# Kernel tuning notes

Hardware: AMD Instinct MI355X
Metric: run time of the kernel (lower is better)

## Reference

```python
import itertools
import jax, jax.numpy as jnp
import numpy as np

B, S, H = 1, 2048, 1024
NH, KVH, HD = 16, 8, 64
E, TOPK, I = 8, 2, 3584
EPS = 1e-6
THETA = 1000000.0
COMBS = np.array(list(itertools.combinations(range(E), TOPK)), dtype=np.int32)  # [28,2]


def setup_inputs() -> dict:
    key = jax.random.key(0)
    ks = jax.random.split(key, 12)
    s = 0.02
    return {
        "hidden_states": jax.random.normal(ks[0], (B, S, H), jnp.float32),
        "ln1_w": jnp.ones((H,), jnp.float32),
        "ln2_w": jnp.ones((H,), jnp.float32),
        "wq": jax.random.normal(ks[1], (NH * HD, H), jnp.float32) * s,
        "wk": jax.random.normal(ks[2], (KVH * HD, H), jnp.float32) * s,
        "wv": jax.random.normal(ks[3], (KVH * HD, H), jnp.float32) * s,
        "wo": jax.random.normal(ks[4], (H, NH * HD), jnp.float32) * s,
        "gate_w": jax.random.normal(ks[5], (E, H), jnp.float32) * s,
        "w1": jax.random.normal(ks[6], (E, I, H), jnp.float32) * s,
        "w2": jax.random.normal(ks[7], (E, H, I), jnp.float32) * s,
        "w3": jax.random.normal(ks[8], (E, I, H), jnp.float32) * s,
    }


def _rmsnorm(x, w):
    v = x.astype(jnp.float32)
    v = v * jax.lax.rsqrt(jnp.mean(v * v, axis=-1, keepdims=True) + EPS)
    return (w * v).astype(x.dtype)


def _rotate_half(x):
    h = x.shape[-1] // 2
    return jnp.concatenate([-x[..., h:], x[..., :h]], axis=-1)


def reference(hidden_states, ln1_w, ln2_w, wq, wk, wv, wo, gate_w, w1, w2, w3):
    residual = hidden_states
    x = _rmsnorm(hidden_states, ln1_w)

    # --- Mixtral attention (GQA + RoPE, causal) ---
    q = (x @ wq.T).reshape(B, S, NH, HD).transpose(0, 2, 1, 3)   # [B,NH,S,HD]
    k = (x @ wk.T).reshape(B, S, KVH, HD).transpose(0, 2, 1, 3)  # [B,KVH,S,HD]
    v = (x @ wv.T).reshape(B, S, KVH, HD).transpose(0, 2, 1, 3)

    pos = jnp.arange(S, dtype=jnp.float32)
    inv_freq = 1.0 / (THETA ** (jnp.arange(0, HD, 2, dtype=jnp.float32) / HD))
    freqs = pos[:, None] * inv_freq[None, :]               # [S,HD/2]
    emb = jnp.concatenate([freqs, freqs], axis=-1)          # [S,HD]
    cos, sin = jnp.cos(emb)[None, None], jnp.sin(emb)[None, None]
    q = q * cos + _rotate_half(q) * sin
    k = k * cos + _rotate_half(k) * sin

    rep = NH // KVH
    k = jnp.repeat(k, rep, axis=1)
    v = jnp.repeat(v, rep, axis=1)

    scores = jnp.einsum("bhsd,bhtd->bhst", q, k) / jnp.sqrt(jnp.float32(HD))
    causal = jnp.tril(jnp.ones((S, S), dtype=bool))
    scores = jnp.where(causal[None, None], scores, jnp.finfo(jnp.float32).min)
    attn = jax.nn.softmax(scores.astype(jnp.float32), axis=-1).astype(q.dtype)
    ctx = jnp.einsum("bhst,bhtd->bhsd", attn, v)
    ctx = ctx.transpose(0, 2, 1, 3).reshape(B, S, NH * HD)
    hidden_states = residual + ctx @ wo.T

    # --- MoE block (combination routing, no experts_used mask) ---
    residual = hidden_states
    x = _rmsnorm(hidden_states, ln2_w).reshape(-1, H)       # [N,H], N=B*S
    N = x.shape[0]
    router_logits = x @ gate_w.T                            # [N,E]
    rw = jax.nn.softmax(router_logits.astype(jnp.float32), axis=-1)

    combs = jnp.asarray(COMBS)                              # [28,2]
    comb_scores = jnp.take(rw, combs, axis=1).sum(-1)       # [N,28]
    sel = jnp.argmax(comb_scores, axis=-1)                  # [N]
    selected_experts = combs[sel]                           # [N,TOPK]
    w = jnp.take_along_axis(rw, selected_experts, axis=1)   # [N,TOPK]
    w = (w / w.sum(-1, keepdims=True)).astype(x.dtype)

    # per-token per-expert combine weights (0 if not selected)
    wm = jnp.zeros((N, E), x.dtype).at[jnp.arange(N)[:, None], selected_experts].set(w)

    # dense evaluation of all experts, combined by sparse weights
    h1 = jax.nn.silu(jnp.einsum("nh,eih->nei", x, w1))
    h3 = jnp.einsum("nh,eih->nei", x, w3)
    out_e = jnp.einsum("nei,ehi->neh", h1 * h3, w2)          # [N,E,H]
    moe_out = jnp.einsum("neh,ne->nh", out_e, wm)

    hidden_states = residual + moe_out.reshape(B, S, H)
    return hidden_states
```

## Files before the change

### kernel.cpp

```cpp
#include <hip/hip_runtime.h>
#include <hip/hip_bf16.h>
#include <math.h>

constexpr int S_ = 2048, H_ = 1024, NH_ = 16, KVH_ = 8, HD_ = 64;
constexpr int E_ = 8, I_ = 3584;
constexpr int KSLC = 4;
constexpr float EPS_ = 1e-6f;
constexpr float THETA_ = 1000000.0f;

#define SDIV(a,b) (((a)+(b)-1)/(b))

typedef __attribute__((ext_vector_type(8))) short bf16x8;
typedef __attribute__((ext_vector_type(4))) float f32x4;

__device__ inline unsigned pkbf(float a, float b) {
    unsigned r;
    asm("v_cvt_pk_bf16_f32 %0, %1, %2" : "=v"(r) : "v"(a), "v"(b));
    return r;
}
__device__ inline unsigned short f2bf(float f) {
    unsigned u = __float_as_uint(f);
    u += 0x7FFF + ((u >> 16) & 1);
    return (unsigned short)(u >> 16);
}
__device__ inline float bf2f(unsigned short v) {
    return __uint_as_float((unsigned)v << 16);
}

__device__ inline void gload16u(const void* gsrc, char* ldsArr, int uoff) {
    int off = __builtin_amdgcn_readfirstlane(uoff);
    __builtin_amdgcn_global_load_lds(
        (__attribute__((address_space(1))) void*)(gsrc),
        (__attribute__((address_space(3))) void*)(ldsArr + off), 16, 0, 0);
}
__device__ inline void vmdrain() {
    asm volatile("s_waitcnt vmcnt(0)" ::: "memory");
}

template<bool WB>
__device__ inline int4 loadW16(const void* W, size_t elemOff) {
    if constexpr (WB) {
        return *(const int4*)((const unsigned short*)W + elemOff);
    } else {
        const float* s = (const float*)W + elemOff;
        float4 f0 = *(const float4*)s, f1 = *(const float4*)(s + 4);
        return make_int4(pkbf(f0.x, f0.y), pkbf(f0.z, f0.w),
                         pkbf(f1.x, f1.y), pkbf(f1.z, f1.w));
    }
}

__global__ __launch_bounds__(256) void conv_bf16(const float* __restrict__ in,
                                                 unsigned short* __restrict__ out, long n8)
{
    long i = (long)blockIdx.x * 256 + threadIdx.x;
    long stride = (long)gridDim.x * 256;
    for (; i < n8; i += stride) {
        const float* s = in + i * 8;
        float4 f0 = *(const float4*)s, f1 = *(const float4*)(s + 4);
        *(int4*)(out + i * 8) = make_int4(pkbf(f0.x, f0.y), pkbf(f0.z, f0.w),
                                          pkbf(f1.x, f1.y), pkbf(f1.z, f1.w));
    }
}

__global__ __launch_bounds__(256) void rmsnorm_k(const float* __restrict__ x,
                                                 const float* __restrict__ w,
                                                 float* __restrict__ out,
                                                 unsigned short* __restrict__ outb)
{
    int row = blockIdx.x;
    int tid = threadIdx.x;
    const float* xr = x + (size_t)row * H_;
    float4 v = *(const float4*)&xr[tid * 4];
    float ss = v.x*v.x + v.y*v.y + v.z*v.z + v.w*v.w;
#pragma unroll
    for (int off = 32; off > 0; off >>= 1) ss += __shfl_xor(ss, off);
    __shared__ float red[4];
    if ((tid & 63) == 0) red[tid >> 6] = ss;
    __syncthreads();
    float tot = red[0] + red[1] + red[2] + red[3];
    float r = rsqrtf(tot / (float)H_ + EPS_);
    float4 wv = *(const float4*)&w[tid * 4];
    float4 o;
    o.x = v.x * r * wv.x; o.y = v.y * r * wv.y;
    o.z = v.z * r * wv.z; o.w = v.w * r * wv.w;
    *(float4*)&out[(size_t)row * H_ + tid * 4] = o;
    if (outb) {
        uint2 pk = make_uint2(pkbf(o.x, o.y), pkbf(o.z, o.w));
        *(uint2*)&outb[(size_t)row * H_ + tid * 4] = pk;
    }
}

template<bool OUTF32>
__global__ __launch_bounds__(256) void dense_g(const unsigned short* __restrict__ A,
                                               const unsigned short* __restrict__ B,
                                               const float* __restrict__ Res,
                                               void* __restrict__ C,
                                               int K, int ldC)
{
    int m0 = blockIdx.y * 128, n0 = blockIdx.x * 64;
    int tid = threadIdx.x;
    __shared__ char As[16384], Bs[8192];
    int lane = tid & 63, w = tid >> 6, wm = w >> 1, wn = w & 1;
    int lm = lane & 15, lk = lane >> 4;
    int wb16 = (tid & ~63) * 16;

    f32x4 z = {0.f, 0.f, 0.f, 0.f};
    f32x4 acc[4][2];
#pragma unroll
    for (int mf = 0; mf < 4; ++mf)
#pragma unroll
        for (int nf = 0; nf < 2; ++nf) acc[mf][nf] = z;

    for (int kt = 0; kt < K / 64; ++kt) {
        int kb = kt * 64;
#pragma unroll
        for (int it = 0; it < 4; ++it) {
            int g = tid + it * 256, row = g >> 3, kg = g & 7;
            int kgs = kg ^ (row & 7);
            gload16u(A + (size_t)(m0 + row) * K + kb + kgs * 8, As, wb16 + it * 4096);
        }
#pragma unroll
        for (int it = 0; it < 2; ++it) {
            int g = tid + it * 256, row = g >> 3, kg = g & 7;
            int kgs = kg ^ (row & 7);
            gload16u(B + (size_t)(n0 + row) * K + kb + kgs * 8, Bs, wb16 + it * 4096);
        }
        vmdrain();
        __syncthreads();
#pragma unroll
        for (int ks = 0; ks < 2; ++ks) {
            bf16x8 af[4];
#pragma unroll
            for (int mf = 0; mf < 4; ++mf) {
                int row = wm * 64 + mf * 16 + lm;
                af[mf] = *(const bf16x8*)(As + row * 128 + ((ks * 64 + lk * 16) ^ ((row & 7) << 4)));
            }
#pragma unroll
            for (int nf = 0; nf < 2; ++nf) {
                int brow = wn * 32 + nf * 16 + lm;
                bf16x8 bf = *(const bf16x8*)(Bs + brow * 128 + ((ks * 64 + lk * 16) ^ ((brow & 7) << 4)));
#pragma unroll
                for (int mf = 0; mf < 4; ++mf)
                    acc[mf][nf] = __builtin_amdgcn_mfma_f32_16x16x32_bf16(af[mf], bf, acc[mf][nf], 0, 0, 0);
            }
        }
        __syncthreads();
    }

#pragma unroll
    for (int mf = 0; mf < 4; ++mf)
#pragma unroll
        for (int nf = 0; nf < 2; ++nf) {
            int col = n0 + wn * 32 + nf * 16 + lm;
#pragma unroll
            for (int j = 0; j < 4; ++j) {
                int row = m0 + wm * 64 + mf * 16 + lk * 4 + j;
                float v = acc[mf][nf][j];
                if constexpr (OUTF32) {
                    float r = Res ? Res[(size_t)row * ldC + col] : 0.0f;
                    ((float*)C)[(size_t)row * ldC + col] = v + r;
                } else {
                    ((unsigned short*)C)[(size_t)row * ldC + col] = f2bf(v);
                }
            }
        }
}

template<bool WB>
__global__ __launch_bounds__(256) void dense_mfma(const float* __restrict__ A,
                                                  const void* __restrict__ Bw,
                                                  const float* __restrict__ Res,
                                                  float* __restrict__ C,
                                                  int M, int N, int K)
{
    __shared__ char As[16384], Bs[16384];
    int tid = threadIdx.x;
    int m0 = blockIdx.y * 128, n0 = blockIdx.x * 128;
    int lane = tid & 63, w = tid >> 6, wm = w >> 1, wn = w & 1;
    int lm = lane & 15, lk = lane >> 4;

    int4 rA[4], rB[4];
    auto loadAll = [&](int kb) {
#pragma unroll
        for (int it = 0; it < 4; ++it) {
            int g = tid + it * 256, row = g >> 3, kg = g & 7;
            const float* s = A + (size_t)(m0 + row) * K + kb + kg * 8;
            float4 f0 = *(const float4*)s, f1 = *(const float4*)(s + 4);
            rA[it] = make_int4(pkbf(f0.x, f0.y), pkbf(f0.z, f0.w),
                               pkbf(f1.x, f1.y), pkbf(f1.z, f1.w));
            rB[it] = loadW16<WB>(Bw, (size_t)(n0 + row) * K + kb + kg * 8);
        }
    };
    auto writeAll = [&]() {
#pragma unroll
        for (int it = 0; it < 4; ++it) {
            int g = tid + it * 256, row = g >> 3, kg = g & 7;
            int byte = row * 128 + ((kg * 16) ^ ((row & 7) << 4));
            *(int4*)(As + byte) = rA[it];
            *(int4*)(Bs + byte) = rB[it];
        }
    };

    f32x4 z = {0.f, 0.f, 0.f, 0.f};
    f32x4 acc[4][4];
#pragma unroll
    for (int mf = 0; mf < 4; ++mf)
#pragma unroll
        for (int nf = 0; nf < 4; ++nf) acc[mf][nf] = z;

    loadAll(0);
    for (int kt = 0; kt < K / 64; ++kt) {
        __syncthreads();
        writeAll();
        __syncthreads();
        if (kt + 1 < K / 64) loadAll((kt + 1) * 64);
#pragma unroll
        for (int ks = 0; ks < 2; ++ks) {
            bf16x8 af[4];
#pragma unroll
            for (int mf = 0; mf < 4; ++mf) {
                int row = wm * 64 + mf * 16 + lm;
                af[mf] = *(const bf16x8*)(As + row * 128 + ((ks * 64 + lk * 16) ^ ((row & 7) << 4)));
            }
#pragma unroll
            for (int nf = 0; nf < 4; ++nf) {
                int brow = wn * 64 + nf * 16 + lm;
                bf16x8 bf = *(const bf16x8*)(Bs + brow * 128 + ((ks * 64 + lk * 16) ^ ((brow & 7) << 4)));
#pragma unroll
                for (int mf = 0; mf < 4; ++mf)
                    acc[mf][nf] = __builtin_amdgcn_mfma_f32_16x16x32_bf16(af[mf], bf, acc[mf][nf], 0, 0, 0);
            }
        }
    }

#pragma unroll
    for (int mf = 0; mf < 4; ++mf)
#pragma unroll
        for (int nf = 0; nf < 4; ++nf) {
            int col = n0 + wn * 64 + nf * 16 + lm;
#pragma unroll
            for (int j = 0; j < 4; ++j) {
                int row = m0 + wm * 64 + mf * 16 + lk * 4 + j;
                float r = Res ? Res[(size_t)row * N + col] : 0.0f;
                C[(size_t)row * N + col] = acc[mf][nf][j] + r;
            }
        }
}

__global__ __launch_bounds__(256) void rope_conv_b(const unsigned short* __restrict__ qkvb,
                                                   unsigned short* __restrict__ qbf,
                                                   unsigned short* __restrict__ kbf)
{
    int idx = blockIdx.x * 256 + threadIdx.x;
    const int totq = S_ * NH_ * 32;
    const int tot = totq + S_ * KVH_ * 32;
    if (idx >= tot) return;
    const unsigned short* src; unsigned short* dst; int s, di; float sc;
    if (idx < totq) {
        s = idx / (NH_ * 32); int r = idx % (NH_ * 32); int h = r >> 5;
        src = qkvb + (size_t)s * 2048 + h * 64;
        dst = qbf + ((size_t)s * NH_ + h) * HD_;
        di = r & 31; sc = 0.125f;
    } else {
        int j2 = idx - totq;
        s = j2 / (KVH_ * 32); int r = j2 % (KVH_ * 32); int kvh = r >> 5;
        src = qkvb + (size_t)s * 2048 + 1024 + kvh * 64;
        dst = kbf + ((size_t)s * KVH_ + kvh) * HD_;
        di = r & 31; sc = 1.0f;
    }
    float invf = powf(THETA_, -(2.0f * di) / (float)HD_);
    float ang = (float)s * invf;
    float c = cosf(ang), sn = sinf(ang);
    float x0 = bf2f(src[di]), x1 = bf2f(src[di + 32]);
    dst[di]      = f2bf((x0 * c - x1 * sn) * sc);
    dst[di + 32] = f2bf((x1 * c + x0 * sn) * sc);
}

__global__ __launch_bounds__(256) void v_trans_b(const unsigned short* __restrict__ qkvb,
                                                 unsigned short* __restrict__ vtb)
{
    int t0 = blockIdx.x * 64, kvh = blockIdx.y;
    __shared__ unsigned short T[64][64];
    int tid = threadIdx.x;
    int k = tid >> 2, d0 = (tid & 3) * 16;
    const unsigned short* src = qkvb + (size_t)(t0 + k) * 2048 + 1536 + kvh * 64 + d0;
    *(int4*)&T[k][d0]     = *(const int4*)(src);
    *(int4*)&T[k][d0 + 8] = *(const int4*)(src + 8);
    __syncthreads();
    int d = tid >> 2, s0 = (tid & 3) * 16;
    unsigned short tmp[16] __attribute__((aligned(16)));
#pragma unroll
    for (int x = 0; x < 16; ++x) {
        int s = s0 + x;
        int key = 16 * (s & 3) + (s >> 2);
        tmp[x] = T[key][d];
    }
    unsigned short* dst = vtb + ((size_t)kvh * HD_ + d) * S_ + t0 + s0;
    *(int4*)(dst)     = *(int4*)(tmp);
    *(int4*)(dst + 8) = *(int4*)(tmp + 8);
}

__global__ __launch_bounds__(256) void rope_conv(const float* __restrict__ q,
                                                 const float* __restrict__ k,
                                                 unsigned short* __restrict__ qbf,
                                                 unsigned short* __restrict__ kbf)
{
    int idx = blockIdx.x * 256 + threadIdx.x;
    const int totq = S_ * NH_ * 32;
    const int tot = totq + S_ * KVH_ * 32;
    if (idx >= tot) return;
    const float* base; unsigned short* obase; int s, di; float sc;
    if (idx < totq) {
        s = idx / (NH_ * 32); int r = idx % (NH_ * 32);
        size_t o = ((size_t)s * NH_ + (r >> 5)) * HD_;
        base = q + o; obase = qbf + o; di = r & 31; sc = 0.125f;
    } else {
        int j2 = idx - totq;
        s = j2 / (KVH_ * 32); int r = j2 % (KVH_ * 32);
        size_t o = ((size_t)s * KVH_ + (r >> 5)) * HD_;
        base = k + o; obase = kbf + o; di = r & 31; sc = 1.0f;
    }
    float invf = powf(THETA_, -(2.0f * di) / (float)HD_);
    float ang = (float)s * invf;
    float c = cosf(ang), sn = sinf(ang);
    float x0 = base[di], x1 = base[di + 32];
    obase[di]      = f2bf((x0 * c - x1 * sn) * sc);
    obase[di + 32] = f2bf((x1 * c + x0 * sn) * sc);
}

__global__ __launch_bounds__(256) void v_trans(const float* __restrict__ v,
                                               unsigned short* __restrict__ vtb)
{
    int t0 = blockIdx.x * 64, kvh = blockIdx.y;
    __shared__ unsigned short T[64][64];
    int tid = threadIdx.x;
    int k = tid >> 2, d0 = (tid & 3) * 16;
    const float* src = v + ((size_t)(t0 + k) * KVH_ + kvh) * HD_ + d0;
#pragma unroll
    for (int x = 0; x < 4; ++x) {
        float4 f = *(const float4*)(src + x * 4);
        T[k][d0 + x*4 + 0] = f2bf(f.x);
        T[k][d0 + x*4 + 1] = f2bf(f.y);
        T[k][d0 + x*4 + 2] = f2bf(f.z);
        T[k][d0 + x*4 + 3] = f2bf(f.w);
    }
    __syncthreads();
    int d = tid >> 2, s0 = (tid & 3) * 16;
    unsigned short tmp[16] __attribute__((aligned(16)));
#pragma unroll
    for (int x = 0; x < 16; ++x) {
        int s = s0 + x;
        int key = 16 * (s & 3) + (s >> 2);
        tmp[x] = T[key][d];
    }
    unsigned short* dst = vtb + ((size_t)kvh * HD_ + d) * S_ + t0 + s0;
    *(int4*)(dst)     = *(int4*)(tmp);
    *(int4*)(dst + 8) = *(int4*)(tmp + 8);
}

__global__ __launch_bounds__(256) void attn_mfma(const unsigned short* __restrict__ qbf,
                                                 const unsigned short* __restrict__ kbf,
                                                 const unsigned short* __restrict__ vtb,
                                                 float* __restrict__ ctx,
                                                 unsigned short* __restrict__ ctxb)
{
    __shared__ char Ps[4 * 2048];
    int pair = blockIdx.x, h = blockIdx.y, z = blockIdx.z;
    int qb = z ? (31 - pair) : pair;
    int q0 = qb * 64;
    int kvh = h >> 1;
    int tid = threadIdx.x;
    int w = tid >> 6, lane = tid & 63;
    int lm = lane & 15, lk = lane >> 4;
    char* myP = Ps + w * 2048;

    bf16x8 qf[2];
    const unsigned short* qrow = qbf + ((size_t)(q0 + w * 16 + lm) * NH_ + h) * HD_;
#pragma unroll
    for (int ks = 0; ks < 2; ++ks)
        qf[ks] = *(const bf16x8*)(qrow + ks * 32 + lk * 8);

    float m_[4], l_[4];
    f32x4 o_[4];
#pragma unroll
    for (int j = 0; j < 4; ++j) { m_[j] = -1e30f; l_[j] = 0.f; }
    f32x4 zf = {0.f, 0.f, 0.f, 0.f};
#pragma unroll
    for (int nd = 0; nd < 4; ++nd) o_[nd] = zf;

    for (int t0 = 0; t0 <= q0; t0 += 64) {
        f32x4 s[4];
#pragma unroll
        for (int nf = 0; nf < 4; ++nf) {
            const unsigned short* krow = kbf + ((size_t)(t0 + nf * 16 + lm) * KVH_ + kvh) * HD_;
            bf16x8 k0 = *(const bf16x8*)(krow + lk * 8);
            bf16x8 k1 = *(const bf16x8*)(krow + 32 + lk * 8);
            f32x4 acc = zf;
            acc = __builtin_amdgcn_mfma_f32_16x16x32_bf16(qf[0], k0, acc, 0, 0, 0);
            acc = __builtin_amdgcn_mfma_f32_16x16x32_bf16(qf[1], k1, acc, 0, 0, 0);
            s[nf] = acc;
        }
        if (t0 == q0) {
#pragma unroll
            for (int nf = 0; nf < 4; ++nf)
#pragma unroll
                for (int j = 0; j < 4; ++j) {
                    int key = nf * 16 + lm, qq = w * 16 + lk * 4 + j;
                    if (key > qq) s[nf][j] = -1e30f;
                }
        }
        float p_[4][4];
#pragma unroll
        for (int j = 0; j < 4; ++j) {
            float mx = fmaxf(fmaxf(s[0][j], s[1][j]), fmaxf(s[2][j], s[3][j]));
#pragma unroll
            for (int off = 8; off > 0; off >>= 1) mx = fmaxf(mx, __shfl_xor(mx, off));
            float nm = fmaxf(m_[j], mx);
            float rs = __expf(m_[j] - nm);
            float sum = 0.f;
#pragma unroll
            for (int nf = 0; nf < 4; ++nf) {
                float pv = __expf(s[nf][j] - nm);
                p_[nf][j] = pv; sum += pv;
            }
#pragma unroll
            for (int off = 8; off > 0; off >>= 1) sum += __shfl_xor(sum, off);
            l_[j] = l_[j] * rs + sum;
            m_[j] = nm;
#pragma unroll
            for (int nd = 0; nd < 4; ++nd) o_[nd][j] *= rs;
        }
#pragma unroll
        for (int j = 0; j < 4; ++j) {
            int r = lk * 4 + j;
            unsigned lo = pkbf(p_[0][j], p_[1][j]);
            unsigned hi = pkbf(p_[2][j], p_[3][j]);
            int byte = (lm * 8) ^ ((r & 7) << 4);
            *(uint2*)(myP + r * 128 + byte) = make_uint2(lo, hi);
        }
#pragma unroll
        for (int ks = 0; ks < 2; ++ks) {
            int byte = (ks * 64 + lk * 16) ^ ((lm & 7) << 4);
            bf16x8 pA = *(const bf16x8*)(myP + lm * 128 + byte);
#pragma unroll
            for (int nd = 0; nd < 4; ++nd) {
                const unsigned short* vrow = vtb + ((size_t)kvh * HD_ + nd * 16 + lm) * S_ + t0 + ks * 32 + lk * 8;
                bf16x8 vB = *(const bf16x8*)vrow;
                o_[nd] = __builtin_amdgcn_mfma_f32_16x16x32_bf16(pA, vB, o_[nd], 0, 0, 0);
            }
        }
    }
#pragma unroll
    for (int nd = 0; nd < 4; ++nd)
#pragma unroll
        for (int j = 0; j < 4; ++j) {
            int r = lk * 4 + j;
            float val = o_[nd][j] / l_[j];
            size_t oidx = ((size_t)(q0 + w * 16 + r) * NH_ + h) * HD_ + nd * 16 + lm;
            ctx[oidx] = val;
            ctxb[oidx] = f2bf(val);
        }
}

__global__ __launch_bounds__(64) void router_k(const float* __restrict__ x2,
                                               const float* __restrict__ gw,
                                               int* __restrict__ cnt,
                                               int* __restrict__ elist,
                                               int* __restrict__ eslot,
                                               float* __restrict__ wslot)
{
    int n = blockIdx.x, lane = threadIdx.x;
    float part[E_];
#pragma unroll
    for (int e = 0; e < E_; ++e) part[e] = 0.f;
    const float* xr = x2 + (size_t)n * H_;
    for (int j = lane; j < H_; j += 64) {
        float xv = xr[j];
#pragma unroll
        for (int e = 0; e < E_; ++e) part[e] = fmaf(xv, gw[e * H_ + j], part[e]);
    }
#pragma unroll
    for (int e = 0; e < E_; ++e)
#pragma unroll
        for (int off = 32; off > 0; off >>= 1) part[e] += __shfl_xor(part[e], off);
    if (lane == 0) {
        float mx = part[0];
#pragma unroll
        for (int e = 1; e < E_; ++e) mx = fmaxf(mx, part[e]);
        float rw[E_]; float ssum = 0.f;
#pragma unroll
        for (int e = 0; e < E_; ++e) { rw[e] = expf(part[e] - mx); ssum += rw[e]; }
#pragma unroll
        for (int e = 0; e < E_; ++e) rw[e] /= ssum;
        float best = -1.f; int ba = 0, bb = 1;
        for (int a = 0; a < E_; ++a)
            for (int b = a + 1; b < E_; ++b) {
                float scv = rw[a] + rw[b];
                if (scv > best) { best = scv; ba = a; bb = b; }
            }
        float wa = rw[ba], wb = rw[bb], wsum = wa + wb;
        wa /= wsum; wb /= wsum;
        int p = atomicAdd(&cnt[ba], 1);
        elist[ba * S_ + p] = n; eslot[ba * S_ + p] = 2 * n;
        p = atomicAdd(&cnt[bb], 1);
        elist[bb * S_ + p] = n; eslot[bb * S_ + p] = 2 * n + 1;
        wslot[2 * n] = wa; wslot[2 * n + 1] = wb;
    }
}

__global__ __launch_bounds__(256) void moe_up_g(const unsigned short* __restrict__ x2b,
                                                const unsigned short* __restrict__ w1b,
                                                const unsigned short* __restrict__ w3b,
                                                const int* __restrict__ cnt,
                                                const int* __restrict__ elist,
                                                const int* __restrict__ eslot,
                                                unsigned short* __restrict__ hbuf)
{
    int e = blockIdx.z;
    int c = cnt[e];
    int p0 = blockIdx.y * 128;
    if (p0 >= c) return;
    int i0 = blockIdx.x * 64;
    int tid = threadIdx.x;

    __shared__ char As[16384], B1s[8192], B3s[8192];
    __shared__ int rowtokS[128], rowslotS[128];
    if (tid < 128) {
        int p = min(p0 + tid, c - 1);
        rowtokS[tid]  = elist[e * S_ + p];
        rowslotS[tid] = eslot[e * S_ + p];
    }
    __syncthreads();

    int lane = tid & 63, w = tid >> 6, wm = w >> 1, wn = w & 1;
    int lm = lane & 15, lk = lane >> 4;
    int wb16 = (tid & ~63) * 16;
    size_t wbase = (size_t)e * I_ * H_;

    f32x4 z = {0.f, 0.f, 0.f, 0.f};
    f32x4 acc1[4][2], acc3[4][2];
#pragma unroll
    for (int mf = 0; mf < 4; ++mf)
#pragma unroll
        for (int nf = 0; nf < 2; ++nf) { acc1[mf][nf] = z; acc3[mf][nf] = z; }

    for (int kt = 0; kt < H_ / 64; ++kt) {
        int kb = kt * 64;
#pragma unroll
        for (int it = 0; it < 4; ++it) {
            int g = tid + it * 256, row = g >> 3, kg = g & 7;
            int kgs = kg ^ (row & 7);
            gload16u(x2b + (size_t)rowtokS[row] * H_ + kb + kgs * 8, As, wb16 + it * 4096);
        }
#pragma unroll
        for (int it = 0; it < 2; ++it) {
            int g = tid + it * 256, row = g >> 3, kg = g & 7;
            int kgs = kg ^ (row & 7);
            size_t off = wbase + (size_t)(i0 + row) * H_ + kb + kgs * 8;
            gload16u(w1b + off, B1s, wb16 + it * 4096);
            gload16u(w3b + off, B3s, wb16 + it * 4096);
        }
        vmdrain();
        __syncthreads();
#pragma unroll
        for (int ks = 0; ks < 2; ++ks) {
            bf16x8 af[4];
#pragma unroll
            for (int mf = 0; mf < 4; ++mf) {
                int row = wm * 64 + mf * 16 + lm;
                af[mf] = *(const bf16x8*)(As + row * 128 + ((ks * 64 + lk * 16) ^ ((row & 7) << 4)));
            }
#pragma unroll
            for (int nf = 0; nf < 2; ++nf) {
                int brow = wn * 32 + nf * 16 + lm;
                int bby = brow * 128 + ((ks * 64 + lk * 16) ^ ((brow & 7) << 4));
                bf16x8 b1 = *(const bf16x8*)(B1s + bby);
                bf16x8 b3 = *(const bf16x8*)(B3s + bby);
#pragma unroll
                for (int mf = 0; mf < 4; ++mf) {
                    acc1[mf][nf] = __builtin_amdgcn_mfma_f32_16x16x32_bf16(af[mf], b1, acc1[mf][nf], 0, 0, 0);
                    acc3[mf][nf] = __builtin_amdgcn_mfma_f32_16x16x32_bf16(af[mf], b3, acc3[mf][nf], 0, 0, 0);
                }
            }
        }
        __syncthreads();
    }

#pragma unroll
    for (int mf = 0; mf < 4; ++mf)
#pragma unroll
        for (int nf = 0; nf < 2; ++nf) {
            int coli = i0 + wn * 32 + nf * 16 + lm;
#pragma unroll
            for (int j = 0; j < 4; ++j) {
                int rloc = wm * 64 + mf * 16 + lk * 4 + j;
                if (p0 + rloc < c) {
                    float h1 = acc1[mf][nf][j];
                    float val = h1 / (1.f + __expf(-h1)) * acc3[mf][nf][j];
                    hbuf[(size_t)rowslotS[rloc] * I_ + coli] = f2bf(val);
                }
            }
        }
}

__global__ __launch_bounds__(256) void moe_dn_g(const unsigned short* __restrict__ hbuf,
                                                const unsigned short* __restrict__ w2b,
                                                const int* __restrict__ cnt,
                                                const int* __restrict__ eslot,
                                                unsigned short* __restrict__ dbuf)
{
    int e = blockIdx.z >> 2;
    int slice = blockIdx.z & 3;
    int c = cnt[e];
    int p0 = blockIdx.y * 128;
    if (p0 >= c) return;
    int h0 = blockIdx.x * 128;
    int tid = threadIdx.x;
    const int kb0 = slice * (I_ / KSLC);

    __shared__ char As[16384], Bs[16384];
    __shared__ int rowslotS[128];
    if (tid < 128) rowslotS[tid] = eslot[e * S_ + min(p0 + tid, c - 1)];
    __syncthreads();

    int lane = tid & 63, w = tid >> 6, wm = w >> 1, wn = w & 1;
    int lm = lane & 15, lk = lane >> 4;
    int wb16 = (tid & ~63) * 16;
    size_t wbase = (size_t)e * H_ * I_;

    f32x4 z = {0.f, 0.f, 0.f, 0.f};
    f32x4 acc[4][4];
#pragma unroll
    for (int mf = 0; mf < 4; ++mf)
#pragma unroll
        for (int nf = 0; nf < 4; ++nf) acc[mf][nf] = z;

    const int NKT = (I_ / KSLC) / 64;
    for (int kt = 0; kt < NKT; ++kt) {
        int kb = kb0 + kt * 64;
#pragma unroll
        for (int it = 0; it < 4; ++it) {
            int g = tid + it * 256, row = g >> 3, kg = g & 7;
            int kgs = kg ^ (row & 7);
            gload16u(hbuf + (size_t)rowslotS[row] * I_ + kb + kgs * 8, As, wb16 + it * 4096);
            gload16u(w2b + wbase + (size_t)(h0 + row) * I_ + kb + kgs * 8, Bs, wb16 + it * 4096);
        }
        vmdrain();
        __syncthreads();
#pragma unroll
        for (int ks = 0; ks < 2; ++ks) {
            bf16x8 af[4];
#pragma unroll
            for (int mf = 0; mf < 4; ++mf) {
                int row = wm * 64 + mf * 16 + lm;
                af[mf] = *(const bf16x8*)(As + row * 128 + ((ks * 64 + lk * 16) ^ ((row & 7) << 4)));
            }
#pragma unroll
            for (int nf = 0; nf < 4; ++nf) {
                int brow = wn * 64 + nf * 16 + lm;
                bf16x8 bf = *(const bf16x8*)(Bs + brow * 128 + ((ks * 64 + lk * 16) ^ ((brow & 7) << 4)));
#pragma unroll
                for (int mf = 0; mf < 4; ++mf)
                    acc[mf][nf] = __builtin_amdgcn_mfma_f32_16x16x32_bf16(af[mf], bf, acc[mf][nf], 0, 0, 0);
            }
        }
        __syncthreads();
    }

    unsigned short* dslice = dbuf + (size_t)slice * S_ * 2 * H_;
#pragma unroll
    for (int mf = 0; mf < 4; ++mf)
#pragma unroll
        for (int nf = 0; nf < 4; ++nf) {
            int colh = h0 + wn * 64 + nf * 16 + lm;
#pragma unroll
            for (int j = 0; j < 4; ++j) {
                int rloc = wm * 64 + mf * 16 + lk * 4 + j;
                if (p0 + rloc < c)
                    dslice[(size_t)rowslotS[rloc] * H_ + colh] = f2bf(acc[mf][nf][j]);
            }
        }
}

template<bool WB>
__global__ __launch_bounds__(256) void moe_up_mfma(const float* __restrict__ x2,
                                                   const void* __restrict__ w1,
                                                   const void* __restrict__ w3,
                                                   const int* __restrict__ cnt,
                                                   const int* __restrict__ elist,
                                                   const int* __restrict__ eslot,
                                                   unsigned short* __restrict__ hbuf)
{
    int e = blockIdx.z;
    int c = cnt[e];
    int p0 = blockIdx.y * 128;
    if (p0 >= c) return;
    int i0 = blockIdx.x * 64;
    int tid = threadIdx.x;

    __shared__ char As[16384], B1s[8192], B3s[8192];
    __shared__ int rowtokS[128], rowslotS[128];
    if (tid < 128) {
        int p = min(p0 + tid, c - 1);
        rowtokS[tid]  = elist[e * S_ + p];
        rowslotS[tid] = eslot[e * S_ + p];
    }
    __syncthreads();

    int lane = tid & 63, w = tid >> 6, wm = w >> 1, wn = w & 1;
    int lm = lane & 15, lk = lane >> 4;
    size_t wbase = (size_t)e * I_ * H_;

    int4 rA[4], rB1[2], rB3[2];
    auto loadAll = [&](int kb) {
#pragma unroll
        for (int it = 0; it < 4; ++it) {
            int g = tid + it * 256, row = g >> 3, kg = g & 7;
            const float* s = x2 + (size_t)rowtokS[row] * H_ + kb + kg * 8;
            float4 f0 = *(const float4*)s, f1 = *(const float4*)(s + 4);
            rA[it] = make_int4(pkbf(f0.x, f0.y), pkbf(f0.z, f0.w),
                               pkbf(f1.x, f1.y), pkbf(f1.z, f1.w));
        }
#pragma unroll
        for (int it = 0; it < 2; ++it) {
            int g = tid + it * 256, row = g >> 3, kg = g & 7;
            size_t off = wbase + (size_t)(i0 + row) * H_ + kb + kg * 8;
            rB1[it] = loadW16<WB>(w1, off);
            rB3[it] = loadW16<WB>(w3, off);
        }
    };
    auto writeAll = [&]() {
#pragma unroll
        for (int it = 0; it < 4; ++it) {
            int g = tid + it * 256, row = g >> 3, kg = g & 7;
            int byte = row * 128 + ((kg * 16) ^ ((row & 7) << 4));
            *(int4*)(As + byte) = rA[it];
        }
#pragma unroll
        for (int it = 0; it < 2; ++it) {
            int g = tid + it * 256, row = g >> 3, kg = g & 7;
            int byte = row * 128 + ((kg * 16) ^ ((row & 7) << 4));
            *(int4*)(B1s + byte) = rB1[it];
            *(int4*)(B3s + byte) = rB3[it];
        }
    };

    f32x4 z = {0.f, 0.f, 0.f, 0.f};
    f32x4 acc1[4][2], acc3[4][2];
#pragma unroll
    for (int mf = 0; mf < 4; ++mf)
#pragma unroll
        for (int nf = 0; nf < 2; ++nf) { acc1[mf][nf] = z; acc3[mf][nf] = z; }

    loadAll(0);
    for (int kt = 0; kt < H_ / 64; ++kt) {
        __syncthreads();
        writeAll();
        __syncthreads();
        if (kt + 1 < H_ / 64) loadAll((kt + 1) * 64);
#pragma unroll
        for (int ks = 0; ks < 2; ++ks) {
            bf16x8 af[4];
#pragma unroll
            for (int mf = 0; mf < 4; ++mf) {
                int row = wm * 64 + mf * 16 + lm;
                af[mf] = *(const bf16x8*)(As + row * 128 + ((ks * 64 + lk * 16) ^ ((row & 7) << 4)));
            }
#pragma unroll
            for (int nf = 0; nf < 2; ++nf) {
                int brow = wn * 32 + nf * 16 + lm;
                int bby = brow * 128 + ((ks * 64 + lk * 16) ^ ((brow & 7) << 4));
                bf16x8 b1 = *(const bf16x8*)(B1s + bby);
                bf16x8 b3 = *(const bf16x8*)(B3s + bby);
#pragma unroll
                for (int mf = 0; mf < 4; ++mf) {
                    acc1[mf][nf] = __builtin_amdgcn_mfma_f32_16x16x32_bf16(af[mf], b1, acc1[mf][nf], 0, 0, 0);
                    acc3[mf][nf] = __builtin_amdgcn_mfma_f32_16x16x32_bf16(af[mf], b3, acc3[mf][nf], 0, 0, 0);
                }
            }
        }
    }

#pragma unroll
    for (int mf = 0; mf < 4; ++mf)
#pragma unroll
        for (int nf = 0; nf < 2; ++nf) {
            int coli = i0 + wn * 32 + nf * 16 + lm;
#pragma unroll
            for (int j = 0; j < 4; ++j) {
                int rloc = wm * 64 + mf * 16 + lk * 4 + j;
                if (p0 + rloc < c) {
                    float h1 = acc1[mf][nf][j];
                    float val = h1 / (1.f + __expf(-h1)) * acc3[mf][nf][j];
                    hbuf[(size_t)rowslotS[rloc] * I_ + coli] = f2bf(val);
                }
            }
        }
}

template<bool WB>
__global__ __launch_bounds__(256) void moe_dn_mfma(const unsigned short* __restrict__ hbuf,
                                                   const void* __restrict__ w2,
                                                   const int* __restrict__ cnt,
                                                   const int* __restrict__ eslot,
                                                   unsigned short* __restrict__ dbuf)
{
    int e = blockIdx.z >> 2;
    int slice = blockIdx.z & 3;
    int c = cnt[e];
    int p0 = blockIdx.y * 128;
    if (p0 >= c) return;
    int h0 = blockIdx.x * 128;
    int tid = threadIdx.x;
    const int kb0 = slice * (I_ / KSLC);

    __shared__ char As[16384], Bs[16384];
    __shared__ int rowslotS[128];
    if (tid < 128) rowslotS[tid] = eslot[e * S_ + min(p0 + tid, c - 1)];
    __syncthreads();

    int lane = tid & 63, w = tid >> 6, wm = w >> 1, wn = w & 1;
    int lm = lane & 15, lk = lane >> 4;
    size_t wbase = (size_t)e * H_ * I_;

    int4 rA[4], rB[4];
    auto loadAll = [&](int kb) {
#pragma unroll
        for (int it = 0; it < 4; ++it) {
            int g = tid + it * 256, row = g >> 3, kg = g & 7;
            rA[it] = *(const int4*)(hbuf + (size_t)rowslotS[row] * I_ + kb + kg * 8);
            rB[it] = loadW16<WB>(w2, wbase + (size_t)(h0 + row) * I_ + kb + kg * 8);
        }
    };
    auto writeAll = [&]() {
#pragma unroll
        for (int it = 0; it < 4; ++it) {
            int g = tid + it * 256, row = g >> 3, kg = g & 7;
            int byte = row * 128 + ((kg * 16) ^ ((row & 7) << 4));
            *(int4*)(As + byte) = rA[it];
            *(int4*)(Bs + byte) = rB[it];
        }
    };

    f32x4 z = {0.f, 0.f, 0.f, 0.f};
    f32x4 acc[4][4];
#pragma unroll
    for (int mf = 0; mf < 4; ++mf)
#pragma unroll
        for (int nf = 0; nf < 4; ++nf) acc[mf][nf] = z;

    loadAll(kb0);
    const int NKT = (I_ / KSLC) / 64;
    for (int kt = 0; kt < NKT; ++kt) {
        __syncthreads();
        writeAll();
        __syncthreads();
        if (kt + 1 < NKT) loadAll(kb0 + (kt + 1) * 64);
#pragma unroll
        for (int ks = 0; ks < 2; ++ks) {
            bf16x8 af[4];
#pragma unroll
            for (int mf = 0; mf < 4; ++mf) {
                int row = wm * 64 + mf * 16 + lm;
                af[mf] = *(const bf16x8*)(As + row * 128 + ((ks * 64 + lk * 16) ^ ((row & 7) << 4)));
            }
#pragma unroll
            for (int nf = 0; nf < 4; ++nf) {
                int brow = wn * 64 + nf * 16 + lm;
                bf16x8 bf = *(const bf16x8*)(Bs + brow * 128 + ((ks * 64 + lk * 16) ^ ((brow & 7) << 4)));
#pragma unroll
                for (int mf = 0; mf < 4; ++mf)
                    acc[mf][nf] = __builtin_amdgcn_mfma_f32_16x16x32_bf16(af[mf], bf, acc[mf][nf], 0, 0, 0);
            }
        }
    }

    unsigned short* dslice = dbuf + (size_t)slice * S_ * 2 * H_;
#pragma unroll
    for (int mf = 0; mf < 4; ++mf)
#pragma unroll
        for (int nf = 0; nf < 4; ++nf) {
            int colh = h0 + wn * 64 + nf * 16 + lm;
#pragma unroll
            for (int j = 0; j < 4; ++j) {
                int rloc = wm * 64 + mf * 16 + lk * 4 + j;
                if (p0 + rloc < c)
                    dslice[(size_t)rowslotS[rloc] * H_ + colh] = f2bf(acc[mf][nf][j]);
            }
        }
}

__global__ __launch_bounds__(256) void combine_k(const float* __restrict__ hid2,
                                                 const unsigned short* __restrict__ dbuf,
                                                 const float* __restrict__ wslot,
                                                 float* __restrict__ out)
{
    int idx = blockIdx.x * 256 + threadIdx.x;
    if (idx >= S_ * H_) return;
    int n = idx >> 10;
    int hcol = idx & (H_ - 1);
    float s0 = 0.f, s1 = 0.f;
#pragma unroll
    for (int sl = 0; sl < KSLC; ++sl) {
        const unsigned short* base = dbuf + (size_t)sl * S_ * 2 * H_;
        s0 += bf2f(base[(size_t)(2 * n)     * H_ + hcol]);
        s1 += bf2f(base[(size_t)(2 * n + 1) * H_ + hcol]);
    }
    out[idx] = hid2[idx] + wslot[2 * n] * s0 + wslot[2 * n + 1] * s1;
}

extern "C" void kernel_launch(void* const* d_in, const int* in_sizes, int n_in,
                              void* d_out, int out_size, void* d_ws, size_t ws_size,
                              hipStream_t stream)
{
    const float* hidden = (const float*)d_in[0];
    const float* ln1    = (const float*)d_in[1];
    const float* ln2    = (const float*)d_in[2];
    const float* wq     = (const float*)d_in[3];
    const float* wk     = (const float*)d_in[4];
    const float* wv     = (const float*)d_in[5];
    const float* wo     = (const float*)d_in[6];
    const float* gw     = (const float*)d_in[7];
    const float* w1     = (const float*)d_in[8];
    const float* w2     = (const float*)d_in[9];
    const float* w3     = (const float*)d_in[10];
    float* out = (float*)d_out;

    char* p = (char*)d_ws;
    auto alignp = [&]() { p = (char*)(((uintptr_t)p + 255) & ~(uintptr_t)255); };
    auto alloc_f = [&](size_t n) { alignp(); float* r = (float*)p; p += n * 4; return r; };
    auto alloc_h = [&](size_t n) { alignp(); unsigned short* r = (unsigned short*)p; p += n * 2; return r; };
    auto alloc_i = [&](size_t n) { alignp(); int* r = (int*)p; p += n * 4; return r; };

    float* xb   = alloc_f((size_t)S_ * H_);
    unsigned short* xbb = alloc_h((size_t)S_ * H_);
    float* q    = alloc_f((size_t)S_ * NH_ * HD_);
    float* kb   = alloc_f((size_t)S_ * KVH_ * HD_);
    float* vb   = alloc_f((size_t)S_ * KVH_ * HD_);
    unsigned short* qkvb = alloc_h((size_t)S_ * 2048);
    float* hid2 = alloc_f((size_t)S_ * H_);
    float* x2   = alloc_f((size_t)S_ * H_);
    unsigned short* x2b  = alloc_h((size_t)S_ * H_);
    unsigned short* ctxb = alloc_h((size_t)S_ * H_);
    unsigned short* hbuf = alloc_h((size_t)S_ * 2 * I_);
    unsigned short* dbuf = alloc_h((size_t)KSLC * S_ * 2 * H_);
    float* wslot= alloc_f((size_t)S_ * 2);
    unsigned short* qbf = alloc_h((size_t)S_ * NH_ * HD_);
    unsigned short* kbf = alloc_h((size_t)S_ * KVH_ * HD_);
    unsigned short* vtb = alloc_h((size_t)KVH_ * HD_ * S_);
    int* cnt   = alloc_i(E_);
    int* elist = alloc_i((size_t)E_ * S_);
    int* eslot = alloc_i((size_t)E_ * S_);
    float* ctx = xb;

    size_t used = (size_t)(p - (char*)d_ws);
    const size_t nW = (size_t)E_ * I_ * H_;
    size_t wbf_bytes = (3 * nW + (size_t)2048 * H_ + (size_t)H_ * NH_ * HD_) * 2 + 8192;
    bool WB = ws_size > used && (ws_size - used) >= wbf_bytes;

    unsigned short *w1b = nullptr, *w3b = nullptr, *w2b = nullptr;
    unsigned short *wqkvb = nullptr, *wob = nullptr;
    if (WB) {
        w1b = alloc_h(nW); w3b = alloc_h(nW); w2b = alloc_h(nW);
        wqkvb = alloc_h((size_t)2048 * H_);
        wob = alloc_h((size_t)H_ * NH_ * HD_);
    }

    hipMemsetAsync(cnt, 0, E_ * sizeof(int), stream);

    if (WB) {
        conv_bf16<<<2048, 256, 0, stream>>>(w1, w1b, (long)(nW / 8));
        conv_bf16<<<2048, 256, 0, stream>>>(w3, w3b, (long)(nW / 8));
        conv_bf16<<<2048, 256, 0, stream>>>(w2, w2b, (long)(nW / 8));
        conv_bf16<<<512, 256, 0, stream>>>(wq, wqkvb, (long)((size_t)NH_*HD_*H_ / 8));
        conv_bf16<<<256, 256, 0, stream>>>(wk, wqkvb + (size_t)NH_*HD_*H_, (long)((size_t)KVH_*HD_*H_ / 8));
        conv_bf16<<<256, 256, 0, stream>>>(wv, wqkvb + (size_t)(NH_+KVH_)*HD_*H_, (long)((size_t)KVH_*HD_*H_ / 8));
        conv_bf16<<<512, 256, 0, stream>>>(wo, wob, (long)((size_t)H_*NH_*HD_ / 8));
    }

    rmsnorm_k<<<S_, 256, 0, stream>>>(hidden, ln1, xb, WB ? xbb : nullptr);

    if (WB) {
        dense_g<false><<<dim3(32, 16), 256, 0, stream>>>(xbb, wqkvb, nullptr, qkvb, H_, 2048);
        {
            int tot = S_ * (NH_ + KVH_) * 32;
            rope_conv_b<<<SDIV(tot, 256), 256, 0, stream>>>(qkvb, qbf, kbf);
        }
        v_trans_b<<<dim3(S_ / 64, KVH_), 256, 0, stream>>>(qkvb, vtb);
        attn_mfma<<<dim3(16, NH_, 2), 256, 0, stream>>>(qbf, kbf, vtb, ctx, ctxb);
        dense_g<true><<<dim3(16, 16), 256, 0, stream>>>(ctxb, wob, hidden, hid2, H_, H_);
    } else {
        dense_mfma<false><<<dim3(8, 16), 256, 0, stream>>>(xb, wq, nullptr, q,  S_, NH_ * HD_, H_);
        dense_mfma<false><<<dim3(4, 16), 256, 0, stream>>>(xb, wk, nullptr, kb, S_, KVH_ * HD_, H_);
        dense_mfma<false><<<dim3(4, 16), 256, 0, stream>>>(xb, wv, nullptr, vb, S_, KVH_ * HD_, H_);
        {
            int tot = S_ * (NH_ + KVH_) * 32;
            rope_conv<<<SDIV(tot, 256), 256, 0, stream>>>(q, kb, qbf, kbf);
        }
        v_trans<<<dim3(S_ / 64, KVH_), 256, 0, stream>>>(vb, vtb);
        attn_mfma<<<dim3(16, NH_, 2), 256, 0, stream>>>(qbf, kbf, vtb, ctx, ctxb);
        dense_mfma<false><<<dim3(8, 16), 256, 0, stream>>>(ctx, wo, hidden, hid2, S_, H_, NH_ * HD_);
    }

    rmsnorm_k<<<S_, 256, 0, stream>>>(hid2, ln2, x2, x2b);
    router_k<<<S_, 64, 0, stream>>>(x2, gw, cnt, elist, eslot, wslot);

    if (WB) {
        moe_up_g<<<dim3(I_ / 64, S_ / 128, E_), 256, 0, stream>>>(x2b, w1b, w3b, cnt, elist, eslot, hbuf);
        moe_dn_g<<<dim3(H_ / 128, S_ / 128, E_ * KSLC), 256, 0, stream>>>(hbuf, w2b, cnt, eslot, dbuf);
    } else {
        moe_up_mfma<false><<<dim3(I_ / 64, S_ / 128, E_), 256, 0, stream>>>(x2, w1, w3, cnt, elist, eslot, hbuf);
        moe_dn_mfma<false><<<dim3(H_ / 128, S_ / 128, E_ * KSLC), 256, 0, stream>>>(hbuf, w2, cnt, eslot, dbuf);
    }
    combine_k<<<SDIV(S_ * H_, 256), 256, 0, stream>>>(hid2, dbuf, wslot, out);
}
```

Before: 467.5 us.

## Double-buffer LDS tiles in MoE up and down GEMM kernels

Both MoE GEMM kernels (up-projection with w1/w3 and down-projection with w2) now keep two LDS buffers. The next K tile is loaded into the spare buffer while MFMAs run on the current one, and one barrier per iteration is removed. The aim is to hide global-to-LDS load latency behind compute. In exchange, LDS use per block doubles (64KB for both kernels), which can lower occupancy. The WAR hazard is covered by the single barrier after vmdrain, since the stage for kt+1 writes the buffer last read in kt-1.

Result: slower. 524.4 us (+12.2%).

```diff
diff --git a/kernel.cpp b/kernel.cpp
--- a/kernel.cpp
+++ b/kernel.cpp
@@ -523,7 +523,7 @@
     int i0 = blockIdx.x * 64;
     int tid = threadIdx.x;
 
-    __shared__ char As[16384], B1s[8192], B3s[8192];
+    __shared__ char As[2][16384], B1s[2][8192], B3s[2][8192];
     __shared__ int rowtokS[128], rowslotS[128];
     if (tid < 128) {
         int p = min(p0 + tid, c - 1);
@@ -537,6 +537,24 @@
     int wb16 = (tid & ~63) * 16;
     size_t wbase = (size_t)e * I_ * H_;
 
+    auto stage = [&](int buf, int kt) {
+        int kb = kt * 64;
+#pragma unroll
+        for (int it = 0; it < 4; ++it) {
+            int g = tid + it * 256, row = g >> 3, kg = g & 7;
+            int kgs = kg ^ (row & 7);
+            gload16u(x2b + (size_t)rowtokS[row] * H_ + kb + kgs * 8, As[buf], wb16 + it * 4096);
+        }
+#pragma unroll
+        for (int it = 0; it < 2; ++it) {
+            int g = tid + it * 256, row = g >> 3, kg = g & 7;
+            int kgs = kg ^ (row & 7);
+            size_t off = wbase + (size_t)(i0 + row) * H_ + kb + kgs * 8;
+            gload16u(w1b + off, B1s[buf], wb16 + it * 4096);
+            gload16u(w3b + off, B3s[buf], wb16 + it * 4096);
+        }
+    };
+
     f32x4 z = {0.f, 0.f, 0.f, 0.f};
     f32x4 acc1[4][2], acc3[4][2];
 #pragma unroll
@@ -544,38 +562,27 @@
 #pragma unroll
         for (int nf = 0; nf < 2; ++nf) { acc1[mf][nf] = z; acc3[mf][nf] = z; }
 
-    for (int kt = 0; kt < H_ / 64; ++kt) {
-        int kb = kt * 64;
-#pragma unroll
-        for (int it = 0; it < 4; ++it) {
-            int g = tid + it * 256, row = g >> 3, kg = g & 7;
-            int kgs = kg ^ (row & 7);
-            gload16u(x2b + (size_t)rowtokS[row] * H_ + kb + kgs * 8, As, wb16 + it * 4096);
-        }
-#pragma unroll
-        for (int it = 0; it < 2; ++it) {
-            int g = tid + it * 256, row = g >> 3, kg = g & 7;
-            int kgs = kg ^ (row & 7);
-            size_t off = wbase + (size_t)(i0 + row) * H_ + kb + kgs * 8;
-            gload16u(w1b + off, B1s, wb16 + it * 4096);
-            gload16u(w3b + off, B3s, wb16 + it * 4096);
-        }
+    stage(0, 0);
+    int cur = 0;
+    const int NKT = H_ / 64;
+    for (int kt = 0; kt < NKT; ++kt) {
         vmdrain();
         __syncthreads();
+        if (kt + 1 < NKT) stage(cur ^ 1, kt + 1);
 #pragma unroll
         for (int ks = 0; ks < 2; ++ks) {
             bf16x8 af[4];
 #pragma unroll
             for (int mf = 0; mf < 4; ++mf) {
                 int row = wm * 64 + mf * 16 + lm;
-                af[mf] = *(const bf16x8*)(As + row * 128 + ((ks * 64 + lk * 16) ^ ((row & 7) << 4)));
+                af[mf] = *(const bf16x8*)(As[cur] + row * 128 + ((ks * 64 + lk * 16) ^ ((row & 7) << 4)));
             }
 #pragma unroll
             for (int nf = 0; nf < 2; ++nf) {
                 int brow = wn * 32 + nf * 16 + lm;
                 int bby = brow * 128 + ((ks * 64 + lk * 16) ^ ((brow & 7) << 4));
-                bf16x8 b1 = *(const bf16x8*)(B1s + bby);
-                bf16x8 b3 = *(const bf16x8*)(B3s + bby);
+                bf16x8 b1 = *(const bf16x8*)(B1s[cur] + bby);
+                bf16x8 b3 = *(const bf16x8*)(B3s[cur] + bby);
 #pragma unroll
                 for (int mf = 0; mf < 4; ++mf) {
                     acc1[mf][nf] = __builtin_amdgcn_mfma_f32_16x16x32_bf16(af[mf], b1, acc1[mf][nf], 0, 0, 0);
@@ -583,7 +590,7 @@
                 }
             }
         }
-        __syncthreads();
+        cur ^= 1;
     }
 
 #pragma unroll
@@ -618,7 +625,7 @@
     int tid = threadIdx.x;
     const int kb0 = slice * (I_ / KSLC);
 
-    __shared__ char As[16384], Bs[16384];
+    __shared__ char As[2][16384], Bs[2][16384];
     __shared__ int rowslotS[128];
     if (tid < 128) rowslotS[tid] = eslot[e * S_ + min(p0 + tid, c - 1)];
     __syncthreads();
@@ -628,6 +635,17 @@
     int wb16 = (tid & ~63) * 16;
     size_t wbase = (size_t)e * H_ * I_;
 
+    auto stage = [&](int buf, int kt) {
+        int kb = kb0 + kt * 64;
+#pragma unroll
+        for (int it = 0; it < 4; ++it) {
+            int g = tid + it * 256, row = g >> 3, kg = g & 7;
+            int kgs = kg ^ (row & 7);
+            gload16u(hbuf + (size_t)rowslotS[row] * I_ + kb + kgs * 8, As[buf], wb16 + it * 4096);
+            gload16u(w2b + wbase + (size_t)(h0 + row) * I_ + kb + kgs * 8, Bs[buf], wb16 + it * 4096);
+        }
+    };
+
     f32x4 z = {0.f, 0.f, 0.f, 0.f};
     f32x4 acc[4][4];
 #pragma unroll
@@ -635,36 +653,31 @@
 #pragma unroll
         for (int nf = 0; nf < 4; ++nf) acc[mf][nf] = z;
 
+    stage(0, 0);
+    int cur = 0;
     const int NKT = (I_ / KSLC) / 64;
     for (int kt = 0; kt < NKT; ++kt) {
-        int kb = kb0 + kt * 64;
-#pragma unroll
-        for (int it = 0; it < 4; ++it) {
-            int g = tid + it * 256, row = g >> 3, kg = g & 7;
-            int kgs = kg ^ (row & 7);
-            gload16u(hbuf + (size_t)rowslotS[row] * I_ + kb + kgs * 8, As, wb16 + it * 4096);
-            gload16u(w2b + wbase + (size_t)(h0 + row) * I_ + kb + kgs * 8, Bs, wb16 + it * 4096);
-        }
         vmdrain();
         __syncthreads();
+        if (kt + 1 < NKT) stage(cur ^ 1, kt + 1);
 #pragma unroll
         for (int ks = 0; ks < 2; ++ks) {
             bf16x8 af[4];
 #pragma unroll
             for (int mf = 0; mf < 4; ++mf) {
                 int row = wm * 64 + mf * 16 + lm;
-                af[mf] = *(const bf16x8*)(As + row * 128 + ((ks * 64 + lk * 16) ^ ((row & 7) << 4)));
+                af[mf] = *(const bf16x8*)(As[cur] + row * 128 + ((ks * 64 + lk * 16) ^ ((row & 7) << 4)));
             }
 #pragma unroll
             for (int nf = 0; nf < 4; ++nf) {
                 int brow = wn * 64 + nf * 16 + lm;
-                bf16x8 bf = *(const bf16x8*)(Bs + brow * 128 + ((ks * 64 + lk * 16) ^ ((brow & 7) << 4)));
+                bf16x8 bf = *(const bf16x8*)(Bs[cur] + brow * 128 + ((ks * 64 + lk * 16) ^ ((brow & 7) << 4)));
 #pragma unroll
                 for (int mf = 0; mf < 4; ++mf)
                     acc[mf][nf] = __builtin_amdgcn_mfma_f32_16x16x32_bf16(af[mf], bf, acc[mf][nf], 0, 0, 0);
             }
         }
-        __syncthreads();
+        cur ^= 1;
     }
 
     unsigned short* dslice = dbuf + (size_t)slice * S_ * 2 * H_;
```
